# Optimization experiments

Hardware: AMD Instinct MI355X
Metric: run time of the kernel (lower is better)

The kernel has to match this reference:

```python
import jax, jax.numpy as jnp
import numpy as np

B, C, H, W = 16, 512, 64, 64
G = 32            # factor; dynamic multinomial group count must equal factor for conv shapes to match
CG = C // G       # channels per group = 16
R = 16            # SE reduction
EPS = 1e-5


def setup_inputs() -> dict:
    key = jax.random.key(0)
    ks = jax.random.split(key, 8)
    n = lambda k, s: jax.random.normal(k, s, dtype=jnp.float32) * 0.05
    return {
        "x": jax.random.normal(ks[0], (B, C, H, W), dtype=jnp.float32),
        # 1x1 conv over cg channels (acts on concatenated pooled h/w strips)
        "w1": n(ks[1], (CG, CG)), "b1": jnp.zeros((CG,), jnp.float32),
        # 3x3 conv over cg channels
        "w3": n(ks[2], (CG, CG, 3, 3)), "b3": jnp.zeros((CG,), jnp.float32),
        # GroupNorm(num_groups=cg, num_channels=cg) affine -> per-channel over HW
        "gn_w": jnp.ones((CG,), jnp.float32), "gn_b": jnp.zeros((CG,), jnp.float32),
        # channel_gate SE (1x1 convs == dense on pooled vector)
        "cg_w1": n(ks[3], (C // R, C)), "cg_b1": jnp.zeros((C // R,), jnp.float32),
        "cg_w2": n(ks[4], (C, C // R)), "cg_b2": jnp.zeros((C,), jnp.float32),
        # global_attn SE
        "ga_w1": n(ks[5], (C // R, C)), "ga_b1": jnp.zeros((C // R,), jnp.float32),
        "ga_w2": n(ks[6], (C, C // R)), "ga_b2": jnp.zeros((C,), jnp.float32),
        # torch init is zeros(1); use 0.5 so the channel branch contributes to output
        "gamma": jnp.full((1,), 0.5, jnp.float32),
    }


def _se(t, wa, ba, wb, bb):
    # AdaptiveAvgPool2d(1) -> 1x1 conv -> ReLU -> 1x1 conv -> sigmoid
    p = t.mean((2, 3))                                  # (b, c)
    hdn = jax.nn.relu(p @ wa.T + ba)                    # (b, c//r)
    return jax.nn.sigmoid(hdn @ wb.T + bb)[:, :, None, None]


def reference(x, w1, b1, w3, b3, gn_w, gn_b, cg_w1, cg_b1, cg_w2, cg_b2,
              ga_w1, ga_b1, ga_w2, ga_b2, gamma):
    b, c, h, w = x.shape
    g, cg = G, c // G
    gx = x.reshape(b * g, cg, h, w)

    # coordinate pooling: (bg, cg, h, 1) and (bg, cg, w, 1)
    xh = gx.mean(3, keepdims=True)
    xw = gx.mean(2, keepdims=True).transpose(0, 1, 3, 2)
    hw = jnp.einsum('oc,bcld->bold', w1, jnp.concatenate([xh, xw], axis=2))
    hw = hw + b1[None, :, None, None]
    xh, xw = hw[:, :, :h], hw[:, :, h:]

    # gated map + per-channel GroupNorm (num_groups == num_channels)
    x1 = gx * jax.nn.sigmoid(xh) * jax.nn.sigmoid(xw.transpose(0, 1, 3, 2))
    mu = x1.mean((2, 3), keepdims=True)
    var = x1.var((2, 3), keepdims=True)
    x1 = (x1 - mu) * jax.lax.rsqrt(var + EPS)
    x1 = x1 * gn_w[None, :, None, None] + gn_b[None, :, None, None]

    # 3x3 conv branch
    x2 = jax.lax.conv_general_dilated(gx, w3, (1, 1), 'SAME',
                                      dimension_numbers=('NCHW', 'OIHW', 'NCHW'))
    x2 = x2 + b3[None, :, None, None]

    # pooled-softmax cross attention: (bg,1,cg) @ (bg,cg,hw)
    a11 = jax.nn.softmax(x1.mean((2, 3)), axis=-1)      # (bg, cg)
    a21 = jax.nn.softmax(x2.mean((2, 3)), axis=-1)
    wv = jnp.einsum('bc,bchw->bhw', a11, x2) + jnp.einsum('bc,bchw->bhw', a21, x1)
    spatial = (gx * jax.nn.sigmoid(wv)[:, None]).reshape(b, c, h, w)

    channel = x * _se(x, cg_w1, cg_b1, cg_w2, cg_b2)
    fused = spatial + gamma * channel
    return fused * _se(fused, ga_w1, ga_b1, ga_w2, ga_b2)
```

## Files before the change

kernel.cpp:

```cpp
#include <hip/hip_runtime.h>
#include <math.h>

#define EPS 1e-5f

typedef float __attribute__((ext_vector_type(4))) floatx4;

__device__ __forceinline__ float sigmoidf_(float v){ return 1.0f/(1.0f+expf(-v)); }

__global__ __launch_bounds__(1024) __attribute__((amdgpu_waves_per_eu(4,4)))
void kAB2(const float* __restrict__ x,
    const float* __restrict__ w1, const float* __restrict__ b1,
    const float* __restrict__ w3, const float* __restrict__ b3,
    const float* __restrict__ gn_w, const float* __restrict__ gn_b,
    float* __restrict__ chansum, float* __restrict__ sigbuf, float* __restrict__ p2part)
{
    const int bg = blockIdx.x;
    const int tid = threadIdx.x;
    const int w = tid >> 6;
    const int lane = tid & 63;

    __shared__ float rs_s[16][64], cs_s[16][64];
    __shared__ float sh_s[16][64], sw_s[16][64];
    __shared__ float chs_s[16], corn_s[16][4], mu_s[16], rstd_s[16];
    __shared__ float w3s[2304], w1s[256], b1s[16];
    __shared__ float regs[144], m2[16], a21_s[16];
    __shared__ float weff_s[144], alpha_s[16], cb_s[2];
    __shared__ float red_s[16][16];

    for (int t=tid; t<2304; t+=1024) w3s[t] = w3[t];
    if (tid < 256) w1s[tid] = w1[tid];
    if (tid < 16)  b1s[tid] = b1[tid];

    const float* xc = x + (((size_t)bg<<4) + w)*4096;
    const float4* xc4 = (const float4*)xc;

    {
        float c0=0.f,c1=0.f,c2=0.f,c3=0.f;
        #pragma unroll
        for (int it=0; it<16; ++it){
            float4 v = xc4[it*64 + lane];
            float rsum = v.x+v.y+v.z+v.w;
            rsum += __shfl_xor(rsum,1); rsum += __shfl_xor(rsum,2);
            rsum += __shfl_xor(rsum,4); rsum += __shfl_xor(rsum,8);
            if ((lane&15)==0) rs_s[w][it*4 + (lane>>4)] = rsum;
            c0+=v.x; c1+=v.y; c2+=v.z; c3+=v.w;
        }
        c0 += __shfl_xor(c0,16); c0 += __shfl_xor(c0,32);
        c1 += __shfl_xor(c1,16); c1 += __shfl_xor(c1,32);
        c2 += __shfl_xor(c2,16); c2 += __shfl_xor(c2,32);
        c3 += __shfl_xor(c3,16); c3 += __shfl_xor(c3,32);
        float tsum = c0+c1+c2+c3;
        tsum += __shfl_xor(tsum,1); tsum += __shfl_xor(tsum,2);
        tsum += __shfl_xor(tsum,4); tsum += __shfl_xor(tsum,8);
        if (lane < 16){
            cs_s[w][lane*4+0]=c0; cs_s[w][lane*4+1]=c1;
            cs_s[w][lane*4+2]=c2; cs_s[w][lane*4+3]=c3;
        }
        if (lane==0){
            chs_s[w]=tsum;
            chansum[(bg<<4)+w]=tsum;
            corn_s[w][0]=xc[0]; corn_s[w][1]=xc[63];
            corn_s[w][2]=xc[4032]; corn_s[w][3]=xc[4095];
        }
    }
    __syncthreads();

    {
        int p  = tid & 127;
        int o0 = tid >> 7;
        bool isrow = (p < 64);
        int pp = p & 63;
        float cat[16];
        #pragma unroll
        for (int cc=0; cc<16; ++cc)
            cat[cc] = (isrow ? rs_s[cc][pp] : cs_s[cc][pp]) * (1.0f/64.0f);
        #pragma unroll
        for (int t2=0; t2<2; ++t2){
            int o = o0 + t2*8;
            float acc = b1s[o];
            #pragma unroll
            for (int cc=0; cc<16; ++cc) acc += w1s[o*16+cc]*cat[cc];
            float sg = sigmoidf_(acc);
            if (isrow) sh_s[o][pp]=sg;
            else       sw_s[o][pp]=sg;
        }
    }
    if (tid < 145){
        float a11[16];
        {
            float mx = gn_b[0];
            #pragma unroll
            for (int i=1;i<16;++i) mx = fmaxf(mx, gn_b[i]);
            float s=0.f;
            #pragma unroll
            for (int i=0;i<16;++i){ a11[i]=expf(gn_b[i]-mx); s+=a11[i]; }
            float inv = 1.0f/s;
            #pragma unroll
            for (int i=0;i<16;++i) a11[i]*=inv;
        }
        if (tid<144){
            float acc=0.f;
            #pragma unroll
            for (int o=0;o<16;++o) acc += a11[o]*w3s[o*144+tid];
            weff_s[tid]=acc;
        } else {
            float acc=0.f;
            #pragma unroll
            for (int o=0;o<16;++o) acc += a11[o]*b3[o];
            cb_s[1]=acc;
        }
    }
    __syncthreads();

    {
        int jb = (lane&15)*4;
        float sw0=sw_s[w][jb], sw1=sw_s[w][jb+1], sw2=sw_s[w][jb+2], sw3=sw_s[w][jb+3];
        float s1=0.f, s2=0.f;
        #pragma unroll
        for (int it=0; it<16; ++it){
            float4 v = xc4[it*64+lane];
            float si = sh_s[w][it*4+(lane>>4)];
            float a0=v.x*si*sw0, a1=v.y*si*sw1, a2=v.z*si*sw2, a3=v.w*si*sw3;
            s1 += a0+a1+a2+a3;
            s2 += a0*a0+a1*a1+a2*a2+a3*a3;
        }
        #pragma unroll
        for (int mm=1;mm<64;mm<<=1){ s1+=__shfl_xor(s1,mm); s2+=__shfl_xor(s2,mm); }
        if (lane==0){
            float mu = s1*(1.0f/4096.0f);
            float var = s2*(1.0f/4096.0f) - mu*mu;
            mu_s[w]=mu; rstd_s[w]=rsqrtf(var+EPS);
        }
    }
    __syncthreads();

    if (tid < 144){
        int c = tid/9, k = tid - c*9, ky = k/3, kx = k - ky*3;
        float r = chs_s[c];
        if (ky==0) r -= rs_s[c][63];
        if (ky==2) r -= rs_s[c][0];
        if (kx==0) r -= cs_s[c][63];
        if (kx==2) r -= cs_s[c][0];
        if (ky!=1 && kx!=1) r += corn_s[c][((ky==0)?2:0)+((kx==0)?1:0)];
        regs[tid] = r;
    }
    __syncthreads();
    if (tid<16){
        float s=0.f;
        const float* wo = w3s + tid*144;
        for (int q=0;q<144;++q) s += wo[q]*regs[q];
        m2[tid] = b3[tid] + s*(1.0f/4096.0f);
    }
    __syncthreads();
    if (tid==0){
        float mx = m2[0];
        for (int i=1;i<16;++i) mx = fmaxf(mx, m2[i]);
        float s=0.f, e[16];
        for (int i=0;i<16;++i){ e[i]=expf(m2[i]-mx); s+=e[i]; }
        for (int i=0;i<16;++i) a21_s[i]=e[i]/s;
    }
    __syncthreads();
    if (tid<16) alpha_s[tid] = a21_s[tid]*gn_w[tid]*rstd_s[tid];
    if (tid==0){
        float cv=0.f;
        for (int c2=0;c2<16;++c2)
            cv += a21_s[c2]*(gn_b[c2] - gn_w[c2]*rstd_s[c2]*mu_s[c2]);
        cb_s[0]=cv;
    }
    __syncthreads();

    {
        const int j = lane;
        const int r0 = __builtin_amdgcn_readfirstlane(4*w);
        const float* xb = x + ((size_t)bg<<4)*4096;
        const float cstv = cb_s[0] + cb_s[1];

        float A0[4], A1[4], A2[4], G[4];
        float keep[16][4];
        #pragma unroll
        for (int r=0;r<4;++r){ A0[r]=0.f; A1[r]=0.f; A2[r]=0.f; G[r]=0.f; }

        #pragma unroll
        for (int c=0;c<16;++c){
            const float* xcc = xb + c*4096;
            float w0=weff_s[c*9+0], w1_=weff_s[c*9+1], w2=weff_s[c*9+2];
            float w3_=weff_s[c*9+3], w4=weff_s[c*9+4], w5=weff_s[c*9+5];
            float w6=weff_s[c*9+6], w7=weff_s[c*9+7], w8=weff_s[c*9+8];
            float alc = alpha_s[c];
            float swv = sw_s[c][j];
            float v[6];
            #pragma unroll
            for (int k=0;k<6;++k){
                int t = r0 - 1 + k;
                int tc = t < 0 ? 0 : (t > 63 ? 63 : t);
                float val = xcc[tc*64 + j];
                v[k] = (t >= 0 && t < 64) ? val : 0.f;
            }
            #pragma unroll
            for (int r=0;r<4;++r) keep[c][r] = v[r+1];
            #pragma unroll
            for (int k=0;k<6;++k){
                if (k<=3){ A0[k]+=w0*v[k]; A1[k]+=w1_*v[k]; A2[k]+=w2*v[k]; }
                if (k>=1 && k<=4){
                    A0[k-1]+=w3_*v[k]; A1[k-1]+=w4*v[k]; A2[k-1]+=w5*v[k];
                    float u = alc * sh_s[c][r0+k-1];
                    G[k-1] += u * (swv * v[k]);
                }
                if (k>=2){ A0[k-2]+=w6*v[k]; A1[k-2]+=w7*v[k]; A2[k-2]+=w8*v[k]; }
            }
        }

        float sg[4];
        #pragma unroll
        for (int r=0;r<4;++r){
            float l = __shfl_up(A0[r], 1);
            if (j==0) l = 0.f;
            float rr = __shfl_down(A2[r], 1);
            if (j==63) rr = 0.f;
            float s = sigmoidf_(l + A1[r] + rr + G[r] + cstv);
            sg[r] = s;
            sigbuf[(size_t)bg*4096 + (r0+r)*64 + j] = s;
        }

        #pragma unroll
        for (int c=0;c<16;++c){
            float acc = keep[c][0]*sg[0] + keep[c][1]*sg[1]
                      + keep[c][2]*sg[2] + keep[c][3]*sg[3];
            #pragma unroll
            for (int mm=1;mm<64;mm<<=1) acc += __shfl_xor(acc, mm);
            if (j==0) red_s[w][c] = acc;
        }
    }
    __syncthreads();
    if (tid<16){
        float tot = 0.f;
        #pragma unroll
        for (int ww=0;ww<16;++ww) tot += red_s[ww][tid];
        p2part[(bg<<4)+tid] = tot;
    }
}

__global__ __launch_bounds__(512) void k_se12(const float* __restrict__ chansum,
    const float* __restrict__ p2part, const float* __restrict__ gamma,
    const float* __restrict__ cg_w1, const float* __restrict__ cg_b1,
    const float* __restrict__ cg_w2, const float* __restrict__ cg_b2,
    const float* __restrict__ ga_w1, const float* __restrict__ ga_b1,
    const float* __restrict__ ga_w2, const float* __restrict__ ga_b2,
    float* __restrict__ se1, float* __restrict__ se2)
{
    int b = blockIdx.x, tid = threadIdx.x;
    __shared__ float pv[512];
    __shared__ float hdn[32];
    __shared__ float se1_s[512];

    float cs_v = chansum[b*512+tid];
    pv[tid] = cs_v*(1.0f/4096.0f);
    __syncthreads();
    if (tid<32){
        float acc = cg_b1[tid];
        const float* wr = cg_w1 + tid*512;
        for (int k=0;k<512;++k) acc += wr[k]*pv[k];
        hdn[tid] = fmaxf(acc, 0.0f);
    }
    __syncthreads();
    {
        float acc = cg_b2[tid];
        const float* wr = cg_w2 + tid*32;
        #pragma unroll
        for (int k=0;k<32;++k) acc += wr[k]*hdn[k];
        float s1v = sigmoidf_(acc);
        se1_s[tid] = s1v;
        se1[b*512+tid] = s1v;
    }
    __syncthreads();
    {
        float praw = p2part[b*512+tid];
        float g0 = gamma[0];
        pv[tid] = (praw + g0*se1_s[tid]*cs_v) * (1.0f/4096.0f);
    }
    __syncthreads();
    if (tid<32){
        float acc = ga_b1[tid];
        const float* wr = ga_w1 + tid*512;
        for (int k=0;k<512;++k) acc += wr[k]*pv[k];
        hdn[tid] = fmaxf(acc, 0.0f);
    }
    __syncthreads();
    {
        float acc = ga_b2[tid];
        const float* wr = ga_w2 + tid*32;
        #pragma unroll
        for (int k=0;k<32;++k) acc += wr[k]*hdn[k];
        se2[b*512+tid] = sigmoidf_(acc);
    }
}

__global__ __launch_bounds__(256) void k7_out(const float* __restrict__ x,
    const float* __restrict__ sigbuf, const float* __restrict__ se1,
    const float* __restrict__ se2, const float* __restrict__ gamma,
    float* __restrict__ out)
{
    const floatx4* x4 = (const floatx4*)x;
    const floatx4* s4 = (const floatx4*)sigbuf;
    floatx4* o4 = (floatx4*)out;
    float g0 = gamma[0];
    int idx = blockIdx.x*256 + threadIdx.x;
    int stride = gridDim.x*256;
    for (int g4 = idx; g4 < 8388608; g4 += stride){
        int e = g4 << 2;
        int bC = e >> 12;
        int pix4 = g4 & 1023;
        int bg = bC >> 4;
        floatx4 xv = x4[g4];
        floatx4 sg = s4[bg*1024 + pix4];
        float f1 = g0*se1[bC];
        float s2v = se2[bC];
        floatx4 ov;
        ov.x = xv.x*(sg.x+f1)*s2v;
        ov.y = xv.y*(sg.y+f1)*s2v;
        ov.z = xv.z*(sg.z+f1)*s2v;
        ov.w = xv.w*(sg.w+f1)*s2v;
        __builtin_nontemporal_store(ov, &o4[g4]);
    }
}

extern "C" void kernel_launch(void* const* d_in, const int* in_sizes, int n_in,
                              void* d_out, int out_size, void* d_ws, size_t ws_size,
                              hipStream_t stream)
{
    const float* x     = (const float*)d_in[0];
    const float* w1    = (const float*)d_in[1];
    const float* b1    = (const float*)d_in[2];
    const float* w3    = (const float*)d_in[3];
    const float* b3    = (const float*)d_in[4];
    const float* gn_w  = (const float*)d_in[5];
    const float* gn_b  = (const float*)d_in[6];
    const float* cg_w1 = (const float*)d_in[7];
    const float* cg_b1 = (const float*)d_in[8];
    const float* cg_w2 = (const float*)d_in[9];
    const float* cg_b2 = (const float*)d_in[10];
    const float* ga_w1 = (const float*)d_in[11];
    const float* ga_b1 = (const float*)d_in[12];
    const float* ga_w2 = (const float*)d_in[13];
    const float* ga_b2 = (const float*)d_in[14];
    const float* gamma = (const float*)d_in[15];
    float* out = (float*)d_out;
    float* ws  = (float*)d_ws;

    float* chansum = ws + 0;
    float* p2part  = ws + 8192;
    float* se1     = ws + 16384;
    float* se2     = ws + 24576;
    float* sigbuf  = ws + 32768;

    kAB2<<<512,1024,0,stream>>>(x, w1, b1, w3, b3, gn_w, gn_b, chansum, sigbuf, p2part);
    k_se12<<<16,512,0,stream>>>(chansum, p2part, gamma, cg_w1, cg_b1, cg_w2, cg_b2,
                                ga_w1, ga_b1, ga_w2, ga_b2, se1, se2);
    k7_out<<<8192,256,0,stream>>>(x, sigbuf, se1, se2, gamma, out);
}
```

Before: 144.4 us.

## Fuse GroupNorm statistics pass into 3x3 conv sweep over rows

Removes the separate per-channel pass that re-read each channel's 4096 values to compute GroupNorm mean and variance. Those statistics are now computed from the row-tile values already loaded for the 3x3 conv accumulation, reduced across lanes per channel and then across waves through shared memory. The G accumulation is moved to a second loop over the kept registers, once alpha (which depends on rstd) is available. This saves a full read of x per block and one barrier, in exchange for 16 per-channel wave reductions inside the conv loop and extra shared arrays.

```diff
diff --git a/kernel.cpp b/kernel.cpp
--- a/kernel.cpp
+++ b/kernel.cpp
@@ -8,7 +8,7 @@
 __device__ __forceinline__ float sigmoidf_(float v){ return 1.0f/(1.0f+expf(-v)); }
 
 __global__ __launch_bounds__(1024) __attribute__((amdgpu_waves_per_eu(4,4)))
-void kAB2(const float* __restrict__ x,
+void kAB3(const float* __restrict__ x,
     const float* __restrict__ w1, const float* __restrict__ b1,
     const float* __restrict__ w3, const float* __restrict__ b3,
     const float* __restrict__ gn_w, const float* __restrict__ gn_b,
@@ -21,11 +21,11 @@
 
     __shared__ float rs_s[16][64], cs_s[16][64];
     __shared__ float sh_s[16][64], sw_s[16][64];
-    __shared__ float chs_s[16], corn_s[16][4], mu_s[16], rstd_s[16];
+    __shared__ float chs_s[16], corn_s[16][4];
     __shared__ float w3s[2304], w1s[256], b1s[16];
     __shared__ float regs[144], m2[16], a21_s[16];
     __shared__ float weff_s[144], alpha_s[16], cb_s[2];
-    __shared__ float red_s[16][16];
+    __shared__ float red_s[16][16], s1red[16][16], s2red[16][16];
 
     for (int t=tid; t<2304; t+=1024) w3s[t] = w3[t];
     if (tid < 256) w1s[tid] = w1[tid];
@@ -110,30 +110,6 @@
             cb_s[1]=acc;
         }
     }
-    __syncthreads();
-
-    {
-        int jb = (lane&15)*4;
-        float sw0=sw_s[w][jb], sw1=sw_s[w][jb+1], sw2=sw_s[w][jb+2], sw3=sw_s[w][jb+3];
-        float s1=0.f, s2=0.f;
-        #pragma unroll
-        for (int it=0; it<16; ++it){
-            float4 v = xc4[it*64+lane];
-            float si = sh_s[w][it*4+(lane>>4)];
-            float a0=v.x*si*sw0, a1=v.y*si*sw1, a2=v.z*si*sw2, a3=v.w*si*sw3;
-            s1 += a0+a1+a2+a3;
-            s2 += a0*a0+a1*a1+a2*a2+a3*a3;
-        }
-        #pragma unroll
-        for (int mm=1;mm<64;mm<<=1){ s1+=__shfl_xor(s1,mm); s2+=__shfl_xor(s2,mm); }
-        if (lane==0){
-            float mu = s1*(1.0f/4096.0f);
-            float var = s2*(1.0f/4096.0f) - mu*mu;
-            mu_s[w]=mu; rstd_s[w]=rsqrtf(var+EPS);
-        }
-    }
-    __syncthreads();
-
     if (tid < 144){
         int c = tid/9, k = tid - c*9, ky = k/3, kx = k - ky*3;
         float r = chs_s[c];
@@ -145,6 +121,7 @@
         regs[tid] = r;
     }
     __syncthreads();
+
     if (tid<16){
         float s=0.f;
         const float* wo = w3s + tid*144;
@@ -152,6 +129,7 @@
         m2[tid] = b3[tid] + s*(1.0f/4096.0f);
     }
     __syncthreads();
+
     if (tid==0){
         float mx = m2[0];
         for (int i=1;i<16;++i) mx = fmaxf(mx, m2[i]);
@@ -159,57 +137,84 @@
         for (int i=0;i<16;++i){ e[i]=expf(m2[i]-mx); s+=e[i]; }
         for (int i=0;i<16;++i) a21_s[i]=e[i]/s;
     }
-    __syncthreads();
-    if (tid<16) alpha_s[tid] = a21_s[tid]*gn_w[tid]*rstd_s[tid];
+
+    const int j = lane;
+    const int r0 = __builtin_amdgcn_readfirstlane(4*w);
+    const float* xb = x + ((size_t)bg<<4)*4096;
+
+    float A0[4], A1[4], A2[4];
+    float keep[16][4];
+    #pragma unroll
+    for (int r=0;r<4;++r){ A0[r]=0.f; A1[r]=0.f; A2[r]=0.f; }
+
+    #pragma unroll
+    for (int c=0;c<16;++c){
+        const float* xcc = xb + c*4096;
+        float w0=weff_s[c*9+0], w1_=weff_s[c*9+1], w2=weff_s[c*9+2];
+        float w3_=weff_s[c*9+3], w4=weff_s[c*9+4], w5=weff_s[c*9+5];
+        float w6=weff_s[c*9+6], w7=weff_s[c*9+7], w8=weff_s[c*9+8];
+        float swv = sw_s[c][j];
+        float v[6];
+        #pragma unroll
+        for (int k=0;k<6;++k){
+            int t = r0 - 1 + k;
+            int tc = t < 0 ? 0 : (t > 63 ? 63 : t);
+            float val = xcc[tc*64 + j];
+            v[k] = (t >= 0 && t < 64) ? val : 0.f;
+        }
+        #pragma unroll
+        for (int r=0;r<4;++r) keep[c][r] = v[r+1];
+        #pragma unroll
+        for (int k=0;k<6;++k){
+            if (k<=3){ A0[k]+=w0*v[k]; A1[k]+=w1_*v[k]; A2[k]+=w2*v[k]; }
+            if (k>=1 && k<=4){ A0[k-1]+=w3_*v[k]; A1[k-1]+=w4*v[k]; A2[k-1]+=w5*v[k]; }
+            if (k>=2){ A0[k-2]+=w6*v[k]; A1[k-2]+=w7*v[k]; A2[k-2]+=w8*v[k]; }
+        }
+        float a0_ = v[1]*sh_s[c][r0+0]*swv;
+        float a1_ = v[2]*sh_s[c][r0+1]*swv;
+        float a2_ = v[3]*sh_s[c][r0+2]*swv;
+        float a3_ = v[4]*sh_s[c][r0+3]*swv;
+        float s1c = a0_+a1_+a2_+a3_;
+        float s2c = a0_*a0_+a1_*a1_+a2_*a2_+a3_*a3_;
+        #pragma unroll
+        for (int mm=1;mm<64;mm<<=1){ s1c+=__shfl_xor(s1c,mm); s2c+=__shfl_xor(s2c,mm); }
+        if (j==0){ s1red[w][c]=s1c; s2red[w][c]=s2c; }
+    }
+    __syncthreads();
+
+    if (tid<16){
+        float S1=0.f, S2=0.f;
+        #pragma unroll
+        for (int ww=0;ww<16;++ww){ S1+=s1red[ww][tid]; S2+=s2red[ww][tid]; }
+        float mu = S1*(1.0f/4096.0f);
+        float var = S2*(1.0f/4096.0f) - mu*mu;
+        float rstd = rsqrtf(var+EPS);
+        alpha_s[tid] = a21_s[tid]*gn_w[tid]*rstd;
+        m2[tid] = a21_s[tid]*(gn_b[tid] - gn_w[tid]*rstd*mu);
+    }
+    __syncthreads();
     if (tid==0){
         float cv=0.f;
-        for (int c2=0;c2<16;++c2)
-            cv += a21_s[c2]*(gn_b[c2] - gn_w[c2]*rstd_s[c2]*mu_s[c2]);
+        #pragma unroll
+        for (int c2=0;c2<16;++c2) cv += m2[c2];
         cb_s[0]=cv;
     }
     __syncthreads();
 
     {
-        const int j = lane;
-        const int r0 = __builtin_amdgcn_readfirstlane(4*w);
-        const float* xb = x + ((size_t)bg<<4)*4096;
         const float cstv = cb_s[0] + cb_s[1];
-
-        float A0[4], A1[4], A2[4], G[4];
-        float keep[16][4];
-        #pragma unroll
-        for (int r=0;r<4;++r){ A0[r]=0.f; A1[r]=0.f; A2[r]=0.f; G[r]=0.f; }
-
+        float G[4];
+        #pragma unroll
+        for (int r=0;r<4;++r) G[r]=0.f;
         #pragma unroll
         for (int c=0;c<16;++c){
-            const float* xcc = xb + c*4096;
-            float w0=weff_s[c*9+0], w1_=weff_s[c*9+1], w2=weff_s[c*9+2];
-            float w3_=weff_s[c*9+3], w4=weff_s[c*9+4], w5=weff_s[c*9+5];
-            float w6=weff_s[c*9+6], w7=weff_s[c*9+7], w8=weff_s[c*9+8];
             float alc = alpha_s[c];
             float swv = sw_s[c][j];
-            float v[6];
-            #pragma unroll
-            for (int k=0;k<6;++k){
-                int t = r0 - 1 + k;
-                int tc = t < 0 ? 0 : (t > 63 ? 63 : t);
-                float val = xcc[tc*64 + j];
-                v[k] = (t >= 0 && t < 64) ? val : 0.f;
-            }
-            #pragma unroll
-            for (int r=0;r<4;++r) keep[c][r] = v[r+1];
-            #pragma unroll
-            for (int k=0;k<6;++k){
-                if (k<=3){ A0[k]+=w0*v[k]; A1[k]+=w1_*v[k]; A2[k]+=w2*v[k]; }
-                if (k>=1 && k<=4){
-                    A0[k-1]+=w3_*v[k]; A1[k-1]+=w4*v[k]; A2[k-1]+=w5*v[k];
-                    float u = alc * sh_s[c][r0+k-1];
-                    G[k-1] += u * (swv * v[k]);
-                }
-                if (k>=2){ A0[k-2]+=w6*v[k]; A1[k-2]+=w7*v[k]; A2[k-2]+=w8*v[k]; }
-            }
-        }
-
+            G[0] += (alc*sh_s[c][r0+0]) * (swv*keep[c][0]);
+            G[1] += (alc*sh_s[c][r0+1]) * (swv*keep[c][1]);
+            G[2] += (alc*sh_s[c][r0+2]) * (swv*keep[c][2]);
+            G[3] += (alc*sh_s[c][r0+3]) * (swv*keep[c][3]);
+        }
         float sg[4];
         #pragma unroll
         for (int r=0;r<4;++r){
@@ -221,7 +226,6 @@
             sg[r] = s;
             sigbuf[(size_t)bg*4096 + (r0+r)*64 + j] = s;
         }
-
         #pragma unroll
         for (int c=0;c<16;++c){
             float acc = keep[c][0]*sg[0] + keep[c][1]*sg[1]
@@ -353,7 +357,7 @@
     float* se2     = ws + 24576;
     float* sigbuf  = ws + 32768;
 
-    kAB2<<<512,1024,0,stream>>>(x, w1, b1, w3, b3, gn_w, gn_b, chansum, sigbuf, p2part);
+    kAB3<<<512,1024,0,stream>>>(x, w1, b1, w3, b3, gn_w, gn_b, chansum, sigbuf, p2part);
     k_se12<<<16,512,0,stream>>>(chansum, p2part, gamma, cg_w1, cg_b1, cg_w2, cg_b2,
                                 ga_w1, ga_b1, ga_w2, ga_b2, se1, se2);
     k7_out<<<8192,256,0,stream>>>(x, sigbuf, se1, se2, gamma, out);
```

Measured after the change: 255.6 us. 1.77x slower.
